# Kernel tuning notes

Measured on AMD Instinct MI355X. Metric: run time of the kernel, lower is better.

Reference implementation:

```python
import jax, jax.numpy as jnp
import numpy as np

B, S, H, N_IN, N_PROC, R = 4, 1024, 1024, 64, 16, 128

def setup_inputs() -> dict:
    key = jax.random.key(0)
    k0, k1, k2, k3, k4 = jax.random.split(key, 5)
    intermediate = jax.random.normal(k0, (B, S, H), dtype=jnp.float32)
    enriched_activations = jax.random.normal(k1, (B, S, N_IN), dtype=jnp.float32)
    # Conv2d(1 -> N_proc, kernel=(5, N_in)), default PyTorch init scale ~ 1/sqrt(fan_in)
    fan_in = 1 * 5 * N_IN
    conv_w = jax.random.uniform(k2, (N_PROC, 1, 5, N_IN), dtype=jnp.float32,
                                minval=-1.0, maxval=1.0) / np.sqrt(fan_in).astype(np.float32)
    conv_b = jnp.zeros((N_PROC,), dtype=jnp.float32)
    down_proj = 0.02 * jax.random.normal(k3, (N_PROC, H, R), dtype=jnp.float32)
    up_proj = 0.02 * jax.random.normal(k4, (N_PROC, R, H), dtype=jnp.float32)
    return {"intermediate": intermediate, "enriched_activations": enriched_activations,
            "conv_w": conv_w, "conv_b": conv_b, "down_proj": down_proj, "up_proj": up_proj}

def reference(intermediate, enriched_activations, conv_w, conv_b, down_proj, up_proj):
    # act_map: [B, 1, S, N_in]; conv kernel (5, N_in) with padding (2, 0) -> [B, N_proc, S, 1]
    act_map = enriched_activations[:, None, :, :]
    pr = jax.lax.conv_general_dilated(
        act_map, conv_w, window_strides=(1, 1), padding=((2, 2), (0, 0)),
        dimension_numbers=("NCHW", "OIHW", "NCHW"))
    pr = pr + conv_b[None, :, None, None]
    # squeeze width, transpose to [B, S, N_proc], sigmoid gate
    process_activations = jax.nn.sigmoid(jnp.transpose(pr[..., 0], (0, 2, 1)))
    # per-expert low-rank transform
    down = jnp.einsum("bsh,nhr->bsnr", intermediate, down_proj)          # [B,S,N,R]
    transformed = jnp.einsum("bsnr,nrh->bsnh", down, up_proj)            # [B,S,N,H]
    # gate-weighted sum over experts (fuses multiply + sum over n)
    output = jnp.einsum("bsnh,bsn->bsh", transformed, process_activations)
    return (output, process_activations)
```

## Files before the change

### kernel.cpp

```cpp
#include <hip/hip_runtime.h>
#include <hip/hip_fp16.h>

#define T_TOK 4096
#define H_DIM 1024
#define NIN   64
#define NP    16
#define R_DIM 128
#define S_DIM 1024
#define N1    (NP * R_DIM)

typedef _Float16 half8  __attribute__((ext_vector_type(8)));
typedef _Float16 half4v __attribute__((ext_vector_type(4)));
typedef float    floatx16 __attribute__((ext_vector_type(16)));

typedef __attribute__((address_space(3))) unsigned char lds_u8_t;
typedef __attribute__((address_space(1))) unsigned char gbl_u8_t;

__device__ __forceinline__ void g2l16(const void* g, void* l) {
  __builtin_amdgcn_global_load_lds((const gbl_u8_t*)g, (lds_u8_t*)l, 16, 0, 0);
}

template <int BM, int BN, int GATE, int K, int N>
__global__ __launch_bounds__(256)
void gemm_kernel(const _Float16* __restrict__ A, const _Float16* __restrict__ BT,
                 const float* __restrict__ gv, void* __restrict__ Cv) {
  constexpr int BK = 128, NCH = BK / 8;
  constexpr int RPC = 64 / NCH;
  constexpr int WM = BM / 2, WN = BN / 2;
  constexpr int MI = WM / 32, NJ = WN / 32;
  constexpr int CA = BM * BK / 2048, CB = BN * BK / 2048;
  __shared__ __align__(16) char smem[(BM + BN) * BK * 2];
  _Float16* sA = (_Float16*)smem;
  _Float16* sB = (_Float16*)(smem + (size_t)BM * BK * 2);

  const int tid = threadIdx.x, wave = tid >> 6, lane = tid & 63;
  const int bxi = blockIdx.x, byi = blockIdx.y;
  const int m0 = byi * BM, n0 = bxi * BN;
  const int wr = (wave >> 1) * WM, wc = (wave & 1) * WN;
  const int rl = lane >> 4;
  const int ql = lane & 15;
  const int r = lane & 31, kh = lane >> 5;

  floatx16 acc[MI][NJ];
  #pragma unroll
  for (int i = 0; i < MI; ++i)
    #pragma unroll
    for (int j = 0; j < NJ; ++j) acc[i][j] = (floatx16)0.f;

  #pragma unroll
  for (int k0 = 0; k0 < K; k0 += BK) {
    __syncthreads();
    #pragma unroll
    for (int c = 0; c < CA; ++c) {
      const int rowB = wave * CA * RPC + c * RPC;
      const int rowL = rowB + rl;
      const int q = ql ^ (rowL & (NCH - 1));
      g2l16(A + (size_t)(m0 + rowL) * K + k0 + q * 8, sA + (size_t)rowB * BK);
    }
    #pragma unroll
    for (int c = 0; c < CB; ++c) {
      const int rowB = wave * CB * RPC + c * RPC;
      const int rowL = rowB + rl;
      const int q = ql ^ (rowL & (NCH - 1));
      g2l16(BT + (size_t)(n0 + rowL) * K + k0 + q * 8, sB + (size_t)rowB * BK);
    }
    __syncthreads();
    #pragma unroll
    for (int h = 0; h < BK / 16; ++h) {
      const int p8 = ((2 * h + kh) ^ (r & (NCH - 1))) * 8;
      half8 af[MI], bf[NJ];
      #pragma unroll
      for (int i = 0; i < MI; ++i)
        af[i] = *reinterpret_cast<const half8*>(&sA[(wr + i * 32 + r) * BK + p8]);
      #pragma unroll
      for (int j = 0; j < NJ; ++j)
        bf[j] = *reinterpret_cast<const half8*>(&sB[(wc + j * 32 + r) * BK + p8]);
      #pragma unroll
      for (int i = 0; i < MI; ++i)
        #pragma unroll
        for (int j = 0; j < NJ; ++j)
          acc[i][j] = __builtin_amdgcn_mfma_f32_32x32x16_f16(af[i], bf[j], acc[i][j], 0, 0, 0);
    }
  }

  if (GATE) {
    _Float16* C = (_Float16*)Cv;
    #pragma unroll
    for (int i = 0; i < MI; ++i)
      #pragma unroll
      for (int g4 = 0; g4 < 4; ++g4)
        #pragma unroll
        for (int rr = 0; rr < 4; ++rr) {
          const int rowL = wr + i * 32 + rr + 8 * g4 + 4 * kh;
          const float g = gv[(size_t)(m0 + rowL) * NP + bxi];
          #pragma unroll
          for (int j = 0; j < NJ; ++j)
            C[(size_t)(m0 + rowL) * N + n0 + wc + j * 32 + r] =
                (_Float16)(acc[i][j][g4 * 4 + rr] * g);
        }
  } else {
    float* C = (float*)Cv;
    #pragma unroll
    for (int i = 0; i < MI; ++i)
      #pragma unroll
      for (int g4 = 0; g4 < 4; ++g4)
        #pragma unroll
        for (int rr = 0; rr < 4; ++rr) {
          const int rowL = wr + i * 32 + rr + 8 * g4 + 4 * kh;
          #pragma unroll
          for (int j = 0; j < NJ; ++j)
            C[(size_t)(m0 + rowL) * N + n0 + wc + j * 32 + r] = acc[i][j][g4 * 4 + rr];
        }
  }
}

__global__ __launch_bounds__(256)
void prep_kernel(const float* __restrict__ enr, const float* __restrict__ cw,
                 const float* __restrict__ cb, const float* __restrict__ inter,
                 const float* __restrict__ dproj, const float* __restrict__ uproj,
                 float* __restrict__ gates, _Float16* __restrict__ Xh,
                 _Float16* __restrict__ BT1, _Float16* __restrict__ UT) {
  __shared__ __align__(16) char smem[25664];
  const int tid = threadIdx.x;
  const int bx = blockIdx.x, nb = gridDim.x;
  {
    const float4* src = (const float4*)inter;
    half4v* dst = (half4v*)Xh;
    for (int i = bx * 256 + tid; i < T_TOK * H_DIM / 4; i += nb * 256) {
      float4 v = src[i];
      half4v o;
      o[0] = (_Float16)v.x; o[1] = (_Float16)v.y; o[2] = (_Float16)v.z; o[3] = (_Float16)v.w;
      dst[i] = o;
    }
  }
  if (bx < 256) {
    float (*sw)[321] = (float (*)[321])smem;
    float (*se)[NIN] = (float (*)[NIN])(smem + 20544);
    const int t0 = bx * 16;
    const int b = t0 >> 10, s0 = t0 & 1023;
    for (int i = tid; i < NP * 320; i += 256) sw[i / 320][i % 320] = cw[i];
    for (int i = tid; i < 20 * NIN; i += 256) {
      int rr = i >> 6, c = i & 63, s = s0 + rr - 2;
      se[rr][c] = (s >= 0 && s < S_DIM) ? enr[((size_t)b * S_DIM + s) * NIN + c] : 0.f;
    }
    __syncthreads();
    const int lt = tid >> 4, n = tid & 15;
    float acc = cb[n];
    #pragma unroll
    for (int dh = 0; dh < 5; ++dh) {
      const float* wrow = &sw[n][dh * 64];
      const float* erow = se[lt + dh];
      #pragma unroll
      for (int j = 0; j < NIN; ++j) acc += erow[j] * wrow[j];
    }
    gates[(size_t)(t0 + lt) * NP + n] = 1.f / (1.f + expf(-acc));
    __syncthreads();
  }
  for (int u = bx; u < 4096; u += nb) {
    const float* src; _Float16* dst; int rows, cols, bxt, byt;
    if (u < 2048) {
      int n = u >> 7, rem = u & 127;
      src = dproj + (size_t)n * H_DIM * R_DIM;
      dst = BT1 + (size_t)n * R_DIM * H_DIM;
      rows = H_DIM; cols = R_DIM; bxt = rem & 3; byt = rem >> 2;
    } else {
      int u2 = u - 2048;
      src = uproj; dst = UT; rows = N1; cols = H_DIM;
      bxt = u2 & 31; byt = u2 >> 5;
    }
    float (*tile)[33] = (float (*)[33])smem;
    const int c0 = bxt * 32, r0 = byt * 32;
    const int tx = tid & 31, ty = tid >> 5;
    #pragma unroll
    for (int k = 0; k < 32; k += 8)
      tile[ty + k][tx] = src[(size_t)(r0 + ty + k) * cols + c0 + tx];
    __syncthreads();
    #pragma unroll
    for (int k = 0; k < 32; k += 8)
      dst[(size_t)(c0 + ty + k) * rows + r0 + tx] = (_Float16)tile[tx][ty + k];
    __syncthreads();
  }
}

extern "C" void kernel_launch(void* const* d_in, const int* in_sizes, int n_in,
                              void* d_out, int out_size, void* d_ws, size_t ws_size,
                              hipStream_t stream) {
  const float* inter = (const float*)d_in[0];
  const float* enr   = (const float*)d_in[1];
  const float* convw = (const float*)d_in[2];
  const float* convb = (const float*)d_in[3];
  const float* dproj = (const float*)d_in[4];
  const float* uproj = (const float*)d_in[5];
  float* out   = (float*)d_out;
  float* gates = out + (size_t)T_TOK * H_DIM;

  _Float16* Xh  = (_Float16*)d_ws;
  _Float16* BT1 = Xh  + (size_t)T_TOK * H_DIM;
  _Float16* UT  = BT1 + (size_t)N1 * H_DIM;
  _Float16* Dsc = UT  + (size_t)H_DIM * N1;

  prep_kernel<<<8448, 256, 0, stream>>>(enr, convw, convb, inter, dproj, uproj,
                                        gates, Xh, BT1, UT);
  gemm_kernel<128, 128, 1, H_DIM, N1>
      <<<dim3(N1 / 128, T_TOK / 128), 256, 0, stream>>>(Xh, BT1, gates, (void*)Dsc);
  gemm_kernel<64, 128, 0, N1, H_DIM>
      <<<dim3(H_DIM / 128, T_TOK / 64), 256, 0, stream>>>(Dsc, UT, nullptr, (void*)out);
}
```

Before: 146.0 us.

## Double-buffer GEMM K-tiles with async LDS loads and fixed 128x128 tiles

```diff
diff --git a/kernel.cpp b/kernel.cpp
--- a/kernel.cpp
+++ b/kernel.cpp
@@ -20,73 +20,81 @@
   __builtin_amdgcn_global_load_lds((const gbl_u8_t*)g, (lds_u8_t*)l, 16, 0, 0);
 }
 
-template <int BM, int BN, int GATE, int K, int N>
+template <int GATE, int K, int N>
 __global__ __launch_bounds__(256)
 void gemm_kernel(const _Float16* __restrict__ A, const _Float16* __restrict__ BT,
                  const float* __restrict__ gv, void* __restrict__ Cv) {
-  constexpr int BK = 128, NCH = BK / 8;
-  constexpr int RPC = 64 / NCH;
-  constexpr int WM = BM / 2, WN = BN / 2;
-  constexpr int MI = WM / 32, NJ = WN / 32;
-  constexpr int CA = BM * BK / 2048, CB = BN * BK / 2048;
-  __shared__ __align__(16) char smem[(BM + BN) * BK * 2];
-  _Float16* sA = (_Float16*)smem;
-  _Float16* sB = (_Float16*)(smem + (size_t)BM * BK * 2);
+  constexpr int NK = K / 64;
+  __shared__ __align__(16) _Float16 smem[4][64 * 128];
 
   const int tid = threadIdx.x, wave = tid >> 6, lane = tid & 63;
-  const int bxi = blockIdx.x, byi = blockIdx.y;
-  const int m0 = byi * BM, n0 = bxi * BN;
-  const int wr = (wave >> 1) * WM, wc = (wave & 1) * WN;
-  const int rl = lane >> 4;
-  const int ql = lane & 15;
+  const int bxi = blockIdx.x;
+  const int m0 = blockIdx.y * 128, n0 = bxi * 128;
+  const int wr = (wave >> 1) * 64, wc = (wave & 1) * 64;
+  const int rl = lane >> 4, ql = lane & 15;
   const int r = lane & 31, kh = lane >> 5;
 
-  floatx16 acc[MI][NJ];
+  auto stage = [&](const _Float16* __restrict__ base, int off0, int k0,
+                   _Float16* dst) {
+    #pragma unroll
+    for (int c = 0; c < 4; ++c) {
+      const int cc = wave * 4 + c;
+      const int lrow = cc * 4 + rl;
+      const int cl = ql ^ (lrow & 15);
+      const int row = lrow + ((cl >> 3) << 6);
+      g2l16(base + (size_t)(off0 + row) * K + k0 + (cl & 7) * 8, dst + cc * 512);
+    }
+  };
+
+  floatx16 acc[2][2];
   #pragma unroll
-  for (int i = 0; i < MI; ++i)
-    #pragma unroll
-    for (int j = 0; j < NJ; ++j) acc[i][j] = (floatx16)0.f;
-
-  #pragma unroll
-  for (int k0 = 0; k0 < K; k0 += BK) {
-    __syncthreads();
-    #pragma unroll
-    for (int c = 0; c < CA; ++c) {
-      const int rowB = wave * CA * RPC + c * RPC;
-      const int rowL = rowB + rl;
-      const int q = ql ^ (rowL & (NCH - 1));
-      g2l16(A + (size_t)(m0 + rowL) * K + k0 + q * 8, sA + (size_t)rowB * BK);
-    }
-    #pragma unroll
-    for (int c = 0; c < CB; ++c) {
-      const int rowB = wave * CB * RPC + c * RPC;
-      const int rowL = rowB + rl;
-      const int q = ql ^ (rowL & (NCH - 1));
-      g2l16(BT + (size_t)(n0 + rowL) * K + k0 + q * 8, sB + (size_t)rowB * BK);
-    }
-    __syncthreads();
-    #pragma unroll
-    for (int h = 0; h < BK / 16; ++h) {
-      const int p8 = ((2 * h + kh) ^ (r & (NCH - 1))) * 8;
-      half8 af[MI], bf[NJ];
-      #pragma unroll
-      for (int i = 0; i < MI; ++i)
-        af[i] = *reinterpret_cast<const half8*>(&sA[(wr + i * 32 + r) * BK + p8]);
-      #pragma unroll
-      for (int j = 0; j < NJ; ++j)
-        bf[j] = *reinterpret_cast<const half8*>(&sB[(wc + j * 32 + r) * BK + p8]);
-      #pragma unroll
-      for (int i = 0; i < MI; ++i)
+  for (int i = 0; i < 2; ++i)
+    #pragma unroll
+    for (int j = 0; j < 2; ++j) acc[i][j] = (floatx16)0.f;
+
+  _Float16 *cA = smem[0], *nA = smem[1], *cB = smem[2], *nB = smem[3];
+  stage(A, m0, 0, cA);
+  stage(BT, n0, 0, cB);
+
+  #pragma unroll 2
+  for (int k = 0; k < NK; ++k) {
+    if (k + 1 < NK) {
+      stage(A, m0, (k + 1) * 64, nA);
+      stage(BT, n0, (k + 1) * 64, nB);
+      __builtin_amdgcn_s_waitcnt(0xF78);
+    } else {
+      __builtin_amdgcn_s_waitcnt(0xF70);
+    }
+    __builtin_amdgcn_s_barrier();
+    __builtin_amdgcn_sched_barrier(0);
+    #pragma unroll
+    for (int h = 0; h < 4; ++h) {
+      const int pA = (2 * h + kh + ((wave >> 1) << 3)) ^ (r & 15);
+      const int pB = (2 * h + kh + ((wave & 1) << 3)) ^ (r & 15);
+      half8 af[2], bf[2];
+      #pragma unroll
+      for (int i = 0; i < 2; ++i)
+        af[i] = *reinterpret_cast<const half8*>(&cA[(i * 32 + r) * 128 + pA * 8]);
+      #pragma unroll
+      for (int j = 0; j < 2; ++j)
+        bf[j] = *reinterpret_cast<const half8*>(&cB[(j * 32 + r) * 128 + pB * 8]);
+      #pragma unroll
+      for (int i = 0; i < 2; ++i)
         #pragma unroll
-        for (int j = 0; j < NJ; ++j)
+        for (int j = 0; j < 2; ++j)
           acc[i][j] = __builtin_amdgcn_mfma_f32_32x32x16_f16(af[i], bf[j], acc[i][j], 0, 0, 0);
     }
+    __builtin_amdgcn_sched_barrier(0);
+    __builtin_amdgcn_s_barrier();
+    _Float16* t;
+    t = cA; cA = nA; nA = t;
+    t = cB; cB = nB; nB = t;
   }
 
   if (GATE) {
     _Float16* C = (_Float16*)Cv;
     #pragma unroll
-    for (int i = 0; i < MI; ++i)
+    for (int i = 0; i < 2; ++i)
       #pragma unroll
       for (int g4 = 0; g4 < 4; ++g4)
         #pragma unroll
@@ -94,21 +102,21 @@
           const int rowL = wr + i * 32 + rr + 8 * g4 + 4 * kh;
           const float g = gv[(size_t)(m0 + rowL) * NP + bxi];
           #pragma unroll
-          for (int j = 0; j < NJ; ++j)
+          for (int j = 0; j < 2; ++j)
             C[(size_t)(m0 + rowL) * N + n0 + wc + j * 32 + r] =
                 (_Float16)(acc[i][j][g4 * 4 + rr] * g);
         }
   } else {
     float* C = (float*)Cv;
     #pragma unroll
-    for (int i = 0; i < MI; ++i)
+    for (int i = 0; i < 2; ++i)
       #pragma unroll
       for (int g4 = 0; g4 < 4; ++g4)
         #pragma unroll
         for (int rr = 0; rr < 4; ++rr) {
           const int rowL = wr + i * 32 + rr + 8 * g4 + 4 * kh;
           #pragma unroll
-          for (int j = 0; j < NJ; ++j)
+          for (int j = 0; j < 2; ++j)
             C[(size_t)(m0 + rowL) * N + n0 + wc + j * 32 + r] = acc[i][j][g4 * 4 + rr];
         }
   }
@@ -201,8 +209,8 @@
 
   prep_kernel<<<8448, 256, 0, stream>>>(enr, convw, convb, inter, dproj, uproj,
                                         gates, Xh, BT1, UT);
-  gemm_kernel<128, 128, 1, H_DIM, N1>
+  gemm_kernel<1, H_DIM, N1>
       <<<dim3(N1 / 128, T_TOK / 128), 256, 0, stream>>>(Xh, BT1, gates, (void*)Dsc);
-  gemm_kernel<64, 128, 0, N1, H_DIM>
-      <<<dim3(H_DIM / 128, T_TOK / 64), 256, 0, stream>>>(Dsc, UT, nullptr, (void*)out);
-}
+  gemm_kernel<0, N1, H_DIM>
+      <<<dim3(H_DIM / 128, T_TOK / 128), 256, 0, stream>>>(Dsc, UT, nullptr, (void*)out);
+}
```

After: 138.1 us. 5.4% less time.
